# Kernel tuning notes

Hardware: AMD Instinct MI355X
Metric: run time of the kernel (lower is better)

## Reference

```python
import jax, jax.numpy as jnp
import numpy as np

BS, DOP, RAN, AZI, ELE = 2, 32, 128, 128, 32
INTERVAL = 0.1
TAU = 1.0


def setup_inputs() -> dict:
    key = jax.random.key(0)
    ks = jax.random.split(key, 7)
    N = RAN * AZI * ELE
    seg = jax.random.normal(ks[0], (BS, N, 1), jnp.float32)
    flow = jax.random.normal(ks[1], (BS, N, 3), jnp.float32) * 2.0
    x1 = jax.random.normal(ks[2], (BS, DOP, RAN, AZI, ELE), jnp.float32)
    dop_arr = jax.random.normal(ks[3], (BS, DOP), jnp.float32)
    coords = jax.random.uniform(ks[4], (BS, 3, RAN, AZI, ELE), jnp.float32)
    ori = jax.random.normal(ks[5], (BS, 3, RAN, AZI, ELE), jnp.float32)
    u = jax.random.uniform(ks[6], (BS, DOP, RAN, AZI, ELE), jnp.float32,
                           minval=1e-6, maxval=1.0 - 1e-6)
    gumbels = -jnp.log(-jnp.log(u))  # Gumbel(0,1) noise (sampled internally in torch)
    return {"seg": seg, "flow": flow, "x1": x1, "dop_arr": dop_arr,
            "coords": coords, "ori": ori, "gumbels": gumbels}


def _gather3d(vol_flat, z, y, x, H, W):
    # vol_flat: (B, C, D*H*W); z,y,x: (B, D, H, W) int32
    B = vol_flat.shape[0]
    idx = ((z * H + y) * W + x).reshape(B, 1, -1)
    g = jnp.take_along_axis(vol_flat, idx, axis=2)
    return g  # (B, C, N)


def _grid_sample_3d_border(vol, gx, gy, gz):
    # Trilinear grid_sample, padding_mode='border', align_corners=True.
    # vol: (B, C, D, H, W); gx/gy/gz: (B, D, H, W) normalized coords in [-1, 1]
    B, C, D, H, W = vol.shape
    ix = jnp.clip((gx + 1.0) * 0.5 * (W - 1), 0.0, W - 1.0)
    iy = jnp.clip((gy + 1.0) * 0.5 * (H - 1), 0.0, H - 1.0)
    iz = jnp.clip((gz + 1.0) * 0.5 * (D - 1), 0.0, D - 1.0)
    x0f, y0f, z0f = jnp.floor(ix), jnp.floor(iy), jnp.floor(iz)
    wx, wy, wz = ix - x0f, iy - y0f, iz - z0f
    x0 = jnp.clip(x0f.astype(jnp.int32), 0, W - 1)
    y0 = jnp.clip(y0f.astype(jnp.int32), 0, H - 1)
    z0 = jnp.clip(z0f.astype(jnp.int32), 0, D - 1)
    x1 = jnp.clip(x0 + 1, 0, W - 1)
    y1 = jnp.clip(y0 + 1, 0, H - 1)
    z1 = jnp.clip(z0 + 1, 0, D - 1)
    vf = vol.reshape(B, C, -1)
    out = jnp.zeros((B, C, D * H * W), vol.dtype)
    for zc, wzc in ((z0, 1.0 - wz), (z1, wz)):
        for yc, wyc in ((y0, 1.0 - wy), (y1, wy)):
            for xc, wxc in ((x0, 1.0 - wx), (x1, wx)):
                w = (wzc * wyc * wxc).reshape(B, 1, -1)
                out = out + w * _gather3d(vf, zc, yc, xc, H, W)
    return out.reshape(B, C, D, H, W)


def _warp_flowxyz(coords, flo):
    B, C, D, H, W = coords.shape
    zz = jnp.arange(D, dtype=jnp.float32)[:, None, None]
    yy = jnp.arange(H, dtype=jnp.float32)[None, :, None]
    xx = jnp.arange(W, dtype=jnp.float32)[None, None, :]
    # vgrid = base grid + flow, per channel (x, y, z)
    vx = xx + flo[:, 0]
    vy = yy + flo[:, 1]
    vz = zz + flo[:, 2]
    gx = 2.0 * vx / (W - 1) - 1.0
    gy = 2.0 * vy / (H - 1) - 1.0
    gz = 2.0 * vz / (D - 1) - 1.0
    r, a, e = coords[:, 0], coords[:, 1], coords[:, 2]
    ce = jnp.cos(e)
    xyz = jnp.stack([r * ce * jnp.cos(a), r * ce * jnp.sin(a), r * jnp.sin(e)], axis=1)
    xyz_new = _grid_sample_3d_border(xyz, gx, gy, gz)
    return xyz_new - xyz


def reference(seg, flow, x1, dop_arr, coords, ori, gumbels):
    bs, dop, ran, azi, ele = x1.shape
    dop_b = dop_arr.reshape(bs, dop, 1, 1, 1)
    # gumbel_softmax(hard=True): forward value is the hard one-hot
    y_soft = jax.nn.softmax((x1 + gumbels) / TAU, axis=1)
    idx = jnp.argmax(y_soft, axis=1)
    y_hard = jax.nn.one_hot(idx, dop, axis=1, dtype=x1.dtype)
    max_x1 = y_hard + y_soft - jax.lax.stop_gradient(y_soft)  # straight-through
    softmax_x1 = jax.nn.softmax(x1, axis=1)
    x1_dop1 = jnp.sum(max_x1 * dop_b, axis=1, keepdims=True)
    x1_dop2 = jnp.sum(softmax_x1 * dop_b, axis=1, keepdims=True)
    x1_dop = jnp.concatenate([x1_dop1, x1_dop2], axis=1)  # (bs, 2, R, A, E)
    seg_v = jnp.transpose(seg, (0, 2, 1)).reshape(bs, -1, ran, azi, ele)
    flow_v = jnp.transpose(flow, (0, 2, 1)).reshape(bs, -1, ran, azi, ele)
    flow_xyz = _warp_flowxyz(coords, flow_v)
    velo = flow_xyz / INTERVAL
    dop_label = jnp.sum(velo * ori, axis=1, keepdims=True)
    dop_error = (dop_label - x1_dop) ** 2
    seg_label = jax.nn.sigmoid(10.0 * (0.15 - dop_error))
    seg_label = jnp.mean(seg_label, axis=1, keepdims=True)
    seg_sig = jax.nn.sigmoid(seg_v)
    loss = jnp.mean(jnp.abs(seg_sig - seg_label))
    return loss
```

## Files before the change

### kernel.cpp

```cpp
#include <hip/hip_runtime.h>
#include <math.h>

#define BSZ  2
#define DOPN 32
#define RAN  128
#define AZI  128
#define ELE  32
#define NVOX (RAN * AZI * ELE)

__device__ __forceinline__ float sigmoidf_(float t) {
    return 1.0f / (1.0f + __expf(-t));
}

__global__ __launch_bounds__(256) void xyz_precompute(
    const float* __restrict__ coords, float* __restrict__ xyz)
{
    const int n = blockIdx.x * 256 + threadIdx.x;
    const int b = blockIdx.y;
    const float* cb = coords + (size_t)b * 3 * NVOX;
    float r = cb[n];
    float a = cb[NVOX + n];
    float e = cb[2 * NVOX + n];
    float sa, ca, se, ce;
    sincosf(a, &sa, &ca);
    sincosf(e, &se, &ce);
    float* xb = xyz + (size_t)b * 3 * NVOX;
    xb[n]            = r * ce * ca;
    xb[NVOX + n]     = r * ce * sa;
    xb[2 * NVOX + n] = r * se;
}

__global__ __launch_bounds__(256) void seg_dop_loss(
    const float* __restrict__ seg, const float* __restrict__ flow,
    const float* __restrict__ x1, const float* __restrict__ dop_arr,
    const float* __restrict__ ori, const float* __restrict__ gumbels,
    const float* __restrict__ xyz, float* __restrict__ out)
{
    __shared__ float s_dop[DOPN];
    __shared__ float s_wave[4];

    const int b = blockIdx.y;
    if (threadIdx.x < DOPN) s_dop[threadIdx.x] = dop_arr[b * DOPN + threadIdx.x];
    __syncthreads();

    const int n = blockIdx.x * 256 + threadIdx.x;

    const size_t base = (size_t)b * DOPN * NVOX + (size_t)n;
    float xr[DOPN];
    float m_lg = -3.4e38f;
    float m_x  = -3.4e38f;
    int   idx  = 0;
    #pragma unroll
    for (int d = 0; d < DOPN; ++d) {
        float xv = x1[base + (size_t)d * NVOX];
        float gv = gumbels[base + (size_t)d * NVOX];
        xr[d] = xv;
        float lg = xv + gv;
        if (lg > m_lg) { m_lg = lg; idx = d; }
        m_x = fmaxf(m_x, xv);
    }
    float ssum = 0.0f, wsum = 0.0f;
    #pragma unroll
    for (int d = 0; d < DOPN; ++d) {
        float ev = __expf(xr[d] - m_x);
        ssum += ev;
        wsum += ev * s_dop[d];
    }
    const float dop1 = s_dop[idx];
    const float dop2 = wsum / ssum;

    const int xI = n & (ELE - 1);
    const int yI = (n >> 5) & (AZI - 1);
    const int zI = n >> 12;

    const float* fl = flow + ((size_t)b * NVOX + (size_t)n) * 3;
    const float fx = fl[0], fy = fl[1], fz = fl[2];

    const float vx = (float)xI + fx;
    const float vy = (float)yI + fy;
    const float vz = (float)zI + fz;

    const float gx = 2.0f * vx / (float)(ELE - 1) - 1.0f;
    const float gy = 2.0f * vy / (float)(AZI - 1) - 1.0f;
    const float gz = 2.0f * vz / (float)(RAN - 1) - 1.0f;
    const float ix = fminf(fmaxf((gx + 1.0f) * 0.5f * (float)(ELE - 1), 0.0f), (float)(ELE - 1));
    const float iy = fminf(fmaxf((gy + 1.0f) * 0.5f * (float)(AZI - 1), 0.0f), (float)(AZI - 1));
    const float iz = fminf(fmaxf((gz + 1.0f) * 0.5f * (float)(RAN - 1), 0.0f), (float)(RAN - 1));

    const float x0f = floorf(ix), y0f = floorf(iy), z0f = floorf(iz);
    const float wx = ix - x0f, wy = iy - y0f, wz = iz - z0f;
    int x0 = (int)x0f; x0 = x0 < 0 ? 0 : (x0 > ELE - 1 ? ELE - 1 : x0);
    int y0 = (int)y0f; y0 = y0 < 0 ? 0 : (y0 > AZI - 1 ? AZI - 1 : y0);
    int z0 = (int)z0f; z0 = z0 < 0 ? 0 : (z0 > RAN - 1 ? RAN - 1 : z0);
    const int x1c = x0 + 1 > ELE - 1 ? ELE - 1 : x0 + 1;
    const int y1c = y0 + 1 > AZI - 1 ? AZI - 1 : y0 + 1;
    const int z1c = z0 + 1 > RAN - 1 ? RAN - 1 : z0 + 1;

    const float* xb = xyz + (size_t)b * 3 * NVOX;
    const int   zs[2]  = { z0, z1c };
    const int   ys[2]  = { y0, y1c };
    const int   xs[2]  = { x0, x1c };
    const float wzv[2] = { 1.0f - wz, wz };
    const float wyv[2] = { 1.0f - wy, wy };
    const float wxv[2] = { 1.0f - wx, wx };

    float sX = 0.0f, sY = 0.0f, sZ = 0.0f;
    #pragma unroll
    for (int i = 0; i < 2; ++i) {
        #pragma unroll
        for (int j = 0; j < 2; ++j) {
            #pragma unroll
            for (int k = 0; k < 2; ++k) {
                const float w = wzv[i] * wyv[j] * wxv[k];
                const int m = (zs[i] * AZI + ys[j]) * ELE + xs[k];
                sX += w * xb[m];
                sY += w * xb[NVOX + m];
                sZ += w * xb[2 * NVOX + m];
            }
        }
    }

    const float bX = xb[n], bY = xb[NVOX + n], bZ = xb[2 * NVOX + n];
    const float vX = (sX - bX) * 10.0f;
    const float vY = (sY - bY) * 10.0f;
    const float vZ = (sZ - bZ) * 10.0f;

    const float* ob = ori + (size_t)b * 3 * NVOX;
    const float dop_label = vX * ob[n] + vY * ob[NVOX + n] + vZ * ob[2 * NVOX + n];

    float e1 = dop_label - dop1; e1 *= e1;
    float e2 = dop_label - dop2; e2 *= e2;
    const float seg_label = 0.5f * (sigmoidf_(10.0f * (0.15f - e1)) +
                                    sigmoidf_(10.0f * (0.15f - e2)));
    const float seg_sig = sigmoidf_(seg[(size_t)b * NVOX + n]);
    float contrib = fabsf(seg_sig - seg_label);

    #pragma unroll
    for (int off = 32; off > 0; off >>= 1)
        contrib += __shfl_down(contrib, off, 64);
    const int lane = threadIdx.x & 63;
    const int wid  = threadIdx.x >> 6;
    if (lane == 0) s_wave[wid] = contrib;
    __syncthreads();
    if (threadIdx.x == 0) {
        const float bsum = s_wave[0] + s_wave[1] + s_wave[2] + s_wave[3];
        atomicAdd(out, bsum * (1.0f / ((float)BSZ * (float)NVOX)));
    }
}

extern "C" void kernel_launch(void* const* d_in, const int* in_sizes, int n_in,
                              void* d_out, int out_size, void* d_ws, size_t ws_size,
                              hipStream_t stream) {
    const float* seg    = (const float*)d_in[0];
    const float* flow   = (const float*)d_in[1];
    const float* x1     = (const float*)d_in[2];
    const float* dopar  = (const float*)d_in[3];
    const float* coords = (const float*)d_in[4];
    const float* ori    = (const float*)d_in[5];
    const float* gumb   = (const float*)d_in[6];
    float* out = (float*)d_out;
    float* xyz = (float*)d_ws;

    hipMemsetAsync(d_out, 0, sizeof(float) * (size_t)out_size, stream);

    dim3 grid(NVOX / 256, BSZ);
    xyz_precompute<<<grid, 256, 0, stream>>>(coords, xyz);
    seg_dop_loss<<<grid, 256, 0, stream>>>(seg, flow, x1, dopar, ori, gumb, xyz, out);
}
```

Baseline: 348.8 us.

## Process four voxels per thread with float4 loads and single-pass softmax

Each thread now handles four consecutive voxels and loads x1, gumbels, flow, xyz, ori and seg as float4 vectors. The softmax becomes a single pass with no max subtraction, so the 32-entry register array goes away. The precompute kernel is vectorised the same way and uses the fast __sincosf intrinsic. The goal is fewer memory instructions and better bandwidth use on a memory-bound kernel, at the cost of exp overflow risk for large x1 values, reduced sincos precision, and fewer blocks.

```diff
diff --git a/kernel.cpp b/kernel.cpp
--- a/kernel.cpp
+++ b/kernel.cpp
@@ -7,133 +7,167 @@
 #define AZI  128
 #define ELE  32
 #define NVOX (RAN * AZI * ELE)
+#define VPT  4
+#define TPB  256
 
 __device__ __forceinline__ float sigmoidf_(float t) {
     return 1.0f / (1.0f + __expf(-t));
 }
 
-__global__ __launch_bounds__(256) void xyz_precompute(
+__global__ __launch_bounds__(TPB) void xyz_precompute(
     const float* __restrict__ coords, float* __restrict__ xyz)
 {
-    const int n = blockIdx.x * 256 + threadIdx.x;
-    const int b = blockIdx.y;
+    const int n0 = (blockIdx.x * TPB + threadIdx.x) * VPT;
+    const int b  = blockIdx.y;
     const float* cb = coords + (size_t)b * 3 * NVOX;
-    float r = cb[n];
-    float a = cb[NVOX + n];
-    float e = cb[2 * NVOX + n];
-    float sa, ca, se, ce;
-    sincosf(a, &sa, &ca);
-    sincosf(e, &se, &ce);
+    const float4 r4 = *(const float4*)(cb + n0);
+    const float4 a4 = *(const float4*)(cb + NVOX + n0);
+    const float4 e4 = *(const float4*)(cb + 2 * NVOX + n0);
+    const float rr[4] = { r4.x, r4.y, r4.z, r4.w };
+    const float aa[4] = { a4.x, a4.y, a4.z, a4.w };
+    const float ee[4] = { e4.x, e4.y, e4.z, e4.w };
+    float X[4], Y[4], Z[4];
+    #pragma unroll
+    for (int v = 0; v < VPT; ++v) {
+        float sa, ca, se, ce;
+        __sincosf(aa[v], &sa, &ca);
+        __sincosf(ee[v], &se, &ce);
+        X[v] = rr[v] * ce * ca;
+        Y[v] = rr[v] * ce * sa;
+        Z[v] = rr[v] * se;
+    }
     float* xb = xyz + (size_t)b * 3 * NVOX;
-    xb[n]            = r * ce * ca;
-    xb[NVOX + n]     = r * ce * sa;
-    xb[2 * NVOX + n] = r * se;
-}
-
-__global__ __launch_bounds__(256) void seg_dop_loss(
+    *(float4*)(xb + n0)            = make_float4(X[0], X[1], X[2], X[3]);
+    *(float4*)(xb + NVOX + n0)     = make_float4(Y[0], Y[1], Y[2], Y[3]);
+    *(float4*)(xb + 2 * NVOX + n0) = make_float4(Z[0], Z[1], Z[2], Z[3]);
+}
+
+__global__ __launch_bounds__(TPB) void seg_dop_loss(
     const float* __restrict__ seg, const float* __restrict__ flow,
     const float* __restrict__ x1, const float* __restrict__ dop_arr,
     const float* __restrict__ ori, const float* __restrict__ gumbels,
     const float* __restrict__ xyz, float* __restrict__ out)
 {
     __shared__ float s_dop[DOPN];
-    __shared__ float s_wave[4];
+    __shared__ float s_wave[TPB / 64];
 
     const int b = blockIdx.y;
     if (threadIdx.x < DOPN) s_dop[threadIdx.x] = dop_arr[b * DOPN + threadIdx.x];
     __syncthreads();
 
-    const int n = blockIdx.x * 256 + threadIdx.x;
-
-    const size_t base = (size_t)b * DOPN * NVOX + (size_t)n;
-    float xr[DOPN];
-    float m_lg = -3.4e38f;
-    float m_x  = -3.4e38f;
-    int   idx  = 0;
+    const int n0 = (blockIdx.x * TPB + threadIdx.x) * VPT;
+    const size_t base = (size_t)b * DOPN * NVOX + (size_t)n0;
+
+    float m_lg[VPT] = { -3.4e38f, -3.4e38f, -3.4e38f, -3.4e38f };
+    float ssum[VPT] = { 0.f, 0.f, 0.f, 0.f };
+    float wsum[VPT] = { 0.f, 0.f, 0.f, 0.f };
+    int   idx[VPT]  = { 0, 0, 0, 0 };
+
+    #pragma unroll 4
+    for (int d = 0; d < DOPN; ++d) {
+        const float4 xv4 = *(const float4*)(x1      + base + (size_t)d * NVOX);
+        const float4 gv4 = *(const float4*)(gumbels + base + (size_t)d * NVOX);
+        const float dv = s_dop[d];
+        const float xv[4] = { xv4.x, xv4.y, xv4.z, xv4.w };
+        const float gv[4] = { gv4.x, gv4.y, gv4.z, gv4.w };
+        #pragma unroll
+        for (int v = 0; v < VPT; ++v) {
+            const float lg = xv[v] + gv[v];
+            if (lg > m_lg[v]) { m_lg[v] = lg; idx[v] = d; }
+            const float ev = __expf(xv[v]);
+            ssum[v] += ev;
+            wsum[v] += ev * dv;
+        }
+    }
+
+    const float* fl = flow + ((size_t)b * NVOX + (size_t)n0) * 3;
+    float fbuf[12];
+    *(float4*)(fbuf)     = *(const float4*)(fl);
+    *(float4*)(fbuf + 4) = *(const float4*)(fl + 4);
+    *(float4*)(fbuf + 8) = *(const float4*)(fl + 8);
+
+    const float* xb = xyz + (size_t)b * 3 * NVOX;
+    const float4 bX4 = *(const float4*)(xb + n0);
+    const float4 bY4 = *(const float4*)(xb + NVOX + n0);
+    const float4 bZ4 = *(const float4*)(xb + 2 * NVOX + n0);
+    const float bX[4] = { bX4.x, bX4.y, bX4.z, bX4.w };
+    const float bY[4] = { bY4.x, bY4.y, bY4.z, bY4.w };
+    const float bZ[4] = { bZ4.x, bZ4.y, bZ4.z, bZ4.w };
+
+    const float* ob = ori + (size_t)b * 3 * NVOX;
+    const float4 oX4 = *(const float4*)(ob + n0);
+    const float4 oY4 = *(const float4*)(ob + NVOX + n0);
+    const float4 oZ4 = *(const float4*)(ob + 2 * NVOX + n0);
+    const float oX[4] = { oX4.x, oX4.y, oX4.z, oX4.w };
+    const float oY[4] = { oY4.x, oY4.y, oY4.z, oY4.w };
+    const float oZ[4] = { oZ4.x, oZ4.y, oZ4.z, oZ4.w };
+
+    const float4 sg4 = *(const float4*)(seg + (size_t)b * NVOX + n0);
+    const float sg[4] = { sg4.x, sg4.y, sg4.z, sg4.w };
+
+    const int xB = n0 & (ELE - 1);
+    const int yI = (n0 >> 5) & (AZI - 1);
+    const int zI = n0 >> 12;
+
+    float contrib = 0.0f;
     #pragma unroll
-    for (int d = 0; d < DOPN; ++d) {
-        float xv = x1[base + (size_t)d * NVOX];
-        float gv = gumbels[base + (size_t)d * NVOX];
-        xr[d] = xv;
-        float lg = xv + gv;
-        if (lg > m_lg) { m_lg = lg; idx = d; }
-        m_x = fmaxf(m_x, xv);
-    }
-    float ssum = 0.0f, wsum = 0.0f;
-    #pragma unroll
-    for (int d = 0; d < DOPN; ++d) {
-        float ev = __expf(xr[d] - m_x);
-        ssum += ev;
-        wsum += ev * s_dop[d];
-    }
-    const float dop1 = s_dop[idx];
-    const float dop2 = wsum / ssum;
-
-    const int xI = n & (ELE - 1);
-    const int yI = (n >> 5) & (AZI - 1);
-    const int zI = n >> 12;
-
-    const float* fl = flow + ((size_t)b * NVOX + (size_t)n) * 3;
-    const float fx = fl[0], fy = fl[1], fz = fl[2];
-
-    const float vx = (float)xI + fx;
-    const float vy = (float)yI + fy;
-    const float vz = (float)zI + fz;
-
-    const float gx = 2.0f * vx / (float)(ELE - 1) - 1.0f;
-    const float gy = 2.0f * vy / (float)(AZI - 1) - 1.0f;
-    const float gz = 2.0f * vz / (float)(RAN - 1) - 1.0f;
-    const float ix = fminf(fmaxf((gx + 1.0f) * 0.5f * (float)(ELE - 1), 0.0f), (float)(ELE - 1));
-    const float iy = fminf(fmaxf((gy + 1.0f) * 0.5f * (float)(AZI - 1), 0.0f), (float)(AZI - 1));
-    const float iz = fminf(fmaxf((gz + 1.0f) * 0.5f * (float)(RAN - 1), 0.0f), (float)(RAN - 1));
-
-    const float x0f = floorf(ix), y0f = floorf(iy), z0f = floorf(iz);
-    const float wx = ix - x0f, wy = iy - y0f, wz = iz - z0f;
-    int x0 = (int)x0f; x0 = x0 < 0 ? 0 : (x0 > ELE - 1 ? ELE - 1 : x0);
-    int y0 = (int)y0f; y0 = y0 < 0 ? 0 : (y0 > AZI - 1 ? AZI - 1 : y0);
-    int z0 = (int)z0f; z0 = z0 < 0 ? 0 : (z0 > RAN - 1 ? RAN - 1 : z0);
-    const int x1c = x0 + 1 > ELE - 1 ? ELE - 1 : x0 + 1;
-    const int y1c = y0 + 1 > AZI - 1 ? AZI - 1 : y0 + 1;
-    const int z1c = z0 + 1 > RAN - 1 ? RAN - 1 : z0 + 1;
-
-    const float* xb = xyz + (size_t)b * 3 * NVOX;
-    const int   zs[2]  = { z0, z1c };
-    const int   ys[2]  = { y0, y1c };
-    const int   xs[2]  = { x0, x1c };
-    const float wzv[2] = { 1.0f - wz, wz };
-    const float wyv[2] = { 1.0f - wy, wy };
-    const float wxv[2] = { 1.0f - wx, wx };
-
-    float sX = 0.0f, sY = 0.0f, sZ = 0.0f;
-    #pragma unroll
-    for (int i = 0; i < 2; ++i) {
+    for (int v = 0; v < VPT; ++v) {
+        const float vx = (float)(xB + v) + fbuf[3 * v + 0];
+        const float vy = (float)yI       + fbuf[3 * v + 1];
+        const float vz = (float)zI       + fbuf[3 * v + 2];
+
+        const float gx = 2.0f * vx / (float)(ELE - 1) - 1.0f;
+        const float gy = 2.0f * vy / (float)(AZI - 1) - 1.0f;
+        const float gz = 2.0f * vz / (float)(RAN - 1) - 1.0f;
+        const float ix = fminf(fmaxf((gx + 1.0f) * 0.5f * (float)(ELE - 1), 0.0f), (float)(ELE - 1));
+        const float iy = fminf(fmaxf((gy + 1.0f) * 0.5f * (float)(AZI - 1), 0.0f), (float)(AZI - 1));
+        const float iz = fminf(fmaxf((gz + 1.0f) * 0.5f * (float)(RAN - 1), 0.0f), (float)(RAN - 1));
+
+        const float x0f = floorf(ix), y0f = floorf(iy), z0f = floorf(iz);
+        const float wx = ix - x0f, wy = iy - y0f, wz = iz - z0f;
+        int x0 = (int)x0f; x0 = x0 < 0 ? 0 : (x0 > ELE - 1 ? ELE - 1 : x0);
+        int y0 = (int)y0f; y0 = y0 < 0 ? 0 : (y0 > AZI - 1 ? AZI - 1 : y0);
+        int z0 = (int)z0f; z0 = z0 < 0 ? 0 : (z0 > RAN - 1 ? RAN - 1 : z0);
+        const int x1c = x0 + 1 > ELE - 1 ? ELE - 1 : x0 + 1;
+        const int y1c = y0 + 1 > AZI - 1 ? AZI - 1 : y0 + 1;
+        const int z1c = z0 + 1 > RAN - 1 ? RAN - 1 : z0 + 1;
+
+        const int   zs[2]  = { z0, z1c };
+        const int   ys[2]  = { y0, y1c };
+        const int   xs[2]  = { x0, x1c };
+        const float wzv[2] = { 1.0f - wz, wz };
+        const float wyv[2] = { 1.0f - wy, wy };
+        const float wxv[2] = { 1.0f - wx, wx };
+
+        float sX = 0.0f, sY = 0.0f, sZ = 0.0f;
         #pragma unroll
-        for (int j = 0; j < 2; ++j) {
+        for (int i = 0; i < 2; ++i) {
             #pragma unroll
-            for (int k = 0; k < 2; ++k) {
-                const float w = wzv[i] * wyv[j] * wxv[k];
-                const int m = (zs[i] * AZI + ys[j]) * ELE + xs[k];
-                sX += w * xb[m];
-                sY += w * xb[NVOX + m];
-                sZ += w * xb[2 * NVOX + m];
+            for (int j = 0; j < 2; ++j) {
+                #pragma unroll
+                for (int k = 0; k < 2; ++k) {
+                    const float w = wzv[i] * wyv[j] * wxv[k];
+                    const int m = (zs[i] * AZI + ys[j]) * ELE + xs[k];
+                    sX += w * xb[m];
+                    sY += w * xb[NVOX + m];
+                    sZ += w * xb[2 * NVOX + m];
+                }
             }
         }
-    }
-
-    const float bX = xb[n], bY = xb[NVOX + n], bZ = xb[2 * NVOX + n];
-    const float vX = (sX - bX) * 10.0f;
-    const float vY = (sY - bY) * 10.0f;
-    const float vZ = (sZ - bZ) * 10.0f;
-
-    const float* ob = ori + (size_t)b * 3 * NVOX;
-    const float dop_label = vX * ob[n] + vY * ob[NVOX + n] + vZ * ob[2 * NVOX + n];
-
-    float e1 = dop_label - dop1; e1 *= e1;
-    float e2 = dop_label - dop2; e2 *= e2;
-    const float seg_label = 0.5f * (sigmoidf_(10.0f * (0.15f - e1)) +
-                                    sigmoidf_(10.0f * (0.15f - e2)));
-    const float seg_sig = sigmoidf_(seg[(size_t)b * NVOX + n]);
-    float contrib = fabsf(seg_sig - seg_label);
+
+        const float vX = (sX - bX[v]) * 10.0f;
+        const float vY = (sY - bY[v]) * 10.0f;
+        const float vZ = (sZ - bZ[v]) * 10.0f;
+        const float dop_label = vX * oX[v] + vY * oY[v] + vZ * oZ[v];
+
+        const float dop1 = s_dop[idx[v]];
+        const float dop2 = wsum[v] / ssum[v];
+        float e1 = dop_label - dop1; e1 *= e1;
+        float e2 = dop_label - dop2; e2 *= e2;
+        const float seg_label = 0.5f * (sigmoidf_(10.0f * (0.15f - e1)) +
+                                        sigmoidf_(10.0f * (0.15f - e2)));
+        contrib += fabsf(sigmoidf_(sg[v]) - seg_label);
+    }
 
     #pragma unroll
     for (int off = 32; off > 0; off >>= 1)
@@ -143,7 +177,9 @@
     if (lane == 0) s_wave[wid] = contrib;
     __syncthreads();
     if (threadIdx.x == 0) {
-        const float bsum = s_wave[0] + s_wave[1] + s_wave[2] + s_wave[3];
+        float bsum = 0.0f;
+        #pragma unroll
+        for (int w = 0; w < TPB / 64; ++w) bsum += s_wave[w];
         atomicAdd(out, bsum * (1.0f / ((float)BSZ * (float)NVOX)));
     }
 }
@@ -163,7 +199,7 @@
 
     hipMemsetAsync(d_out, 0, sizeof(float) * (size_t)out_size, stream);
 
-    dim3 grid(NVOX / 256, BSZ);
-    xyz_precompute<<<grid, 256, 0, stream>>>(coords, xyz);
-    seg_dop_loss<<<grid, 256, 0, stream>>>(seg, flow, x1, dopar, ori, gumb, xyz, out);
-}
+    dim3 grid(NVOX / (TPB * VPT), BSZ);
+    xyz_precompute<<<grid, TPB, 0, stream>>>(coords, xyz);
+    seg_dop_loss<<<grid, TPB, 0, stream>>>(seg, flow, x1, dopar, ori, gumb, xyz, out);
+}
```

New measurement: 359.1 us. 3.0% more time.
